# Performance work log

Hardware: AMD Instinct MI355X
Metric: run time of the kernel (lower is better)

The kernel has to match this reference:

```python
import jax, jax.numpy as jnp
import numpy as np

B, S, D = 2, 2048, 1024
H, DH = 16, 64  # n_heads, d_head = d_model // n_heads


def setup_inputs() -> dict:
    key = jax.random.key(0)
    ks = jax.random.split(key, 8)
    sc = lambda d: 1.0 / np.sqrt(d)
    return {
        "x": jax.random.normal(ks[0], (B, S, D), jnp.float32),
        "context": jax.random.normal(ks[1], (B, D), jnp.float32),
        "prev_state": jax.random.normal(ks[2], (B, S, D), jnp.float32),
        "attention_mask": jnp.ones((B, 1, S, S), dtype=bool),
        "Wq": jax.random.normal(ks[3], (D, D), jnp.float32) * sc(D),
        "Wk": jax.random.normal(ks[4], (D, D), jnp.float32) * sc(D),
        "Wv": jax.random.normal(ks[5], (D, D), jnp.float32) * sc(D),
        "Wo": jax.random.normal(ks[6], (D, D), jnp.float32) * sc(D),
        "Wc": jax.random.normal(ks[7], (D, DH), jnp.float32) * sc(D),
        "alpha": jnp.ones((1,), jnp.float32),
        "beta": jnp.ones((1,), jnp.float32),
    }


def reference(x, context, prev_state, attention_mask, Wq, Wk, Wv, Wo, Wc, alpha, beta):
    b, s, d = x.shape
    # projections (Linear with no bias, weight stored as [out, in] -> x @ W.T)
    q = (x @ Wq.T).reshape(b, s, H, DH).transpose(0, 2, 1, 3)  # (B,H,S,DH)
    k = (x @ Wk.T).reshape(b, s, H, DH).transpose(0, 2, 1, 3)
    v = (x @ Wv.T).reshape(b, s, H, DH).transpose(0, 2, 1, 3)

    inv_sqrt_dh = 1.0 / jnp.sqrt(jnp.asarray(DH, x.dtype))
    scores = jnp.einsum("bhqd,bhkd->bhqk", q, k) * inv_sqrt_dh

    # CFM: context-flow matching bias, rank-1 per-pair term from global context
    c = context @ Wc  # (B, DH)
    qc = jnp.einsum("bhqd,bd->bhq", q, c)
    kc = jnp.einsum("bhkd,bd->bhk", k, c)
    cfm = qc[..., :, None] * kc[..., None, :] / DH  # (B,H,S,S)

    # AFM: anti-flow matching bias from previous layer state (first d_head dims)
    p = prev_state[..., :DH]  # (B,S,DH)
    afm = jnp.einsum("bhqd,bkd->bhqk", q, p) * inv_sqrt_dh

    scores = scores + alpha[0] * cfm - beta[0] * afm
    scores = jnp.where(attention_mask, scores, jnp.asarray(-1e9, scores.dtype))

    w = jax.nn.softmax(scores, axis=-1)
    out = jnp.einsum("bhqk,bhkd->bhqd", w, v)  # (B,H,S,DH)
    out = out.transpose(0, 2, 1, 3).reshape(b, s, d)
    return out @ Wo.T
```

## Files before the change

kernel.cpp:

```cpp
#include <hip/hip_runtime.h>
#include <stdint.h>

#define D_  1024
#define S_  2048
#define B_  2
#define H_  16
#define DH_ 64
#define M_  (B_*S_)

typedef __bf16 bf16x8 __attribute__((ext_vector_type(8)));
typedef float  f32x4  __attribute__((ext_vector_type(4)));
typedef float  f32x16 __attribute__((ext_vector_type(16)));
typedef short  short8 __attribute__((ext_vector_type(8)));
typedef unsigned uint4v __attribute__((ext_vector_type(4)));
typedef unsigned short u16;

static __device__ __forceinline__ u16 f2bf(float f){
  union { float f; unsigned u; } v; v.f = f;
  unsigned r = v.u + 0x7FFF + ((v.u >> 16) & 1);
  return (u16)(r >> 16);
}
static __device__ __forceinline__ f32x4 mfma16(short8 a, short8 b, f32x4 c){
  return __builtin_amdgcn_mfma_f32_16x16x32_bf16(
      __builtin_bit_cast(bf16x8, a), __builtin_bit_cast(bf16x8, b), c, 0, 0, 0);
}
static __device__ __forceinline__ f32x16 mfma32(short8 a, short8 b, f32x16 c){
  return __builtin_amdgcn_mfma_f32_32x32x16_bf16(
      __builtin_bit_cast(bf16x8, a), __builtin_bit_cast(bf16x8, b), c, 0, 0, 0);
}
static __device__ __forceinline__ f32x16 zero16(){
  f32x16 z = {0,0,0,0,0,0,0,0,0,0,0,0,0,0,0,0};
  return z;
}
static __device__ __forceinline__ float fexp2(float x){
#if __has_builtin(__builtin_amdgcn_exp2f)
  return __builtin_amdgcn_exp2f(x);
#else
  return __exp2f(x);
#endif
}
static __device__ __forceinline__ unsigned cvtpk(float lo, float hi){
  unsigned r;
  asm("v_cvt_pk_bf16_f32 %0, %1, %2" : "=v"(r) : "v"(lo), "v"(hi));
  return r;
}
static __device__ __forceinline__ void gl_lds16(const u16* g, u16* lds){
  __builtin_amdgcn_global_load_lds(
      (const __attribute__((address_space(1))) void*)(uintptr_t)g,
      (__attribute__((address_space(3))) void*)(uintptr_t)lds, 16, 0, 0);
}

__global__ void k_f2bf(const float* __restrict__ in, u16* __restrict__ out, int n4){
  int i = blockIdx.x * blockDim.x + threadIdx.x;
  if(i >= n4) return;
  float4 v = ((const float4*)in)[i];
  ushort4 o; o.x = f2bf(v.x); o.y = f2bf(v.y); o.z = f2bf(v.z); o.w = f2bf(v.w);
  ((ushort4*)out)[i] = o;
}

__global__ void k_f2bf4(const float* __restrict__ a0, const float* __restrict__ a1,
                        const float* __restrict__ a2, const float* __restrict__ a3,
                        u16* __restrict__ o0, u16* __restrict__ o1,
                        u16* __restrict__ o2, u16* __restrict__ o3, int n4){
  const float* in; u16* out;
  switch(blockIdx.y){
    case 0: in=a0; out=o0; break;
    case 1: in=a1; out=o1; break;
    case 2: in=a2; out=o2; break;
    default: in=a3; out=o3; break;
  }
  int i = blockIdx.x * blockDim.x + threadIdx.x;
  if(i >= n4) return;
  float4 v = ((const float4*)in)[i];
  ushort4 o; o.x = f2bf(v.x); o.y = f2bf(v.y); o.z = f2bf(v.z); o.w = f2bf(v.w);
  ((ushort4*)out)[i] = o;
}

__global__ void k_ctx(const float* __restrict__ context, const float* __restrict__ Wc,
                      float* __restrict__ cvec, int* __restrict__ flags){
  __shared__ float partial[4][2][64];
  int t = threadIdx.x;
  if(t < 2) flags[t] = 1;
  int c = t >> 7;
  int b = (t >> 6) & 1;
  int j = t & 63;
  float s = 0.f;
  #pragma unroll 8
  for(int d = c*256; d < (c+1)*256; ++d) s += context[b*D_ + d] * Wc[d*DH_ + j];
  partial[c][b][j] = s;
  __syncthreads();
  if(t < 128){
    int b2 = t >> 6, j2 = t & 63;
    cvec[b2*DH_ + j2] = partial[0][b2][j2] + partial[1][b2][j2]
                      + partial[2][b2][j2] + partial[3][b2][j2];
  }
}

__global__ void k_mask_check(const uint4* __restrict__ m, int n16, int* flags){
  int i = blockIdx.x * blockDim.x + threadIdx.x;
  bool ok8 = true, ok32 = true;
  if(i < n16){
    uint4 v = m[i];
    ok8  = (v.x==0x01010101u)&&(v.y==0x01010101u)&&(v.z==0x01010101u)&&(v.w==0x01010101u);
    ok32 = (v.x==1u)&&(v.y==1u)&&(v.z==1u)&&(v.w==1u);
  }
  unsigned long long b8  = __ballot(!ok8);
  unsigned long long b32 = __ballot(!ok32);
  if((threadIdx.x & 63) == 0){
    if(b8)  flags[0] = 0;
    if(b32) flags[1] = 0;
  }
}

__global__ __launch_bounds__(256,2) void k_gemm_qkv(const u16* __restrict__ A,
    const u16* __restrict__ Wcat, u16* __restrict__ Qb, u16* __restrict__ Kb,
    u16* __restrict__ VT, const float* __restrict__ cvec,
    const float* __restrict__ prev, const float* __restrict__ beta_p,
    float* __restrict__ qcb, float* __restrict__ kcb){
  __shared__ u16 As[128*64];
  __shared__ u16 Bs[128*64];
  __shared__ float red[2][2][64];
  const int tid = threadIdx.x;
  const int w = tid >> 6, l = tid & 63;
  const int wr = w >> 1, wc = w & 1;
  const int id = blockIdx.x;
  const int bn = id >> 5;
  const int bm = id & 31;
  const int lr = l & 15, lh = l >> 4;
  const int srow = l >> 3, scol = (l & 7) * 8;

  f32x4 acc[4][4] = {};

  for(int kt = 0; kt < 16; ++kt){
    const int k0 = kt * 64;
    #pragma unroll
    for(int i = 0; i < 4; ++i){
      const int chunk = i*4 + w;
      gl_lds16(A    + (size_t)(bm*128 + chunk*8 + srow)*D_ + k0 + scol, &As[chunk*512]);
      gl_lds16(Wcat + (size_t)(bn*128 + chunk*8 + srow)*D_ + k0 + scol, &Bs[chunk*512]);
    }
    __syncthreads();
    #pragma unroll
    for(int kk = 0; kk < 2; ++kk){
      short8 a[4], b[4];
      #pragma unroll
      for(int m = 0; m < 4; ++m)
        a[m] = *(const short8*)&As[(wr*64 + m*16 + lr)*64 + kk*32 + lh*8];
      #pragma unroll
      for(int n = 0; n < 4; ++n)
        b[n] = *(const short8*)&Bs[(wc*64 + n*16 + lr)*64 + kk*32 + lh*8];
      #pragma unroll
      for(int m = 0; m < 4; ++m)
        #pragma unroll
        for(int n = 0; n < 4; ++n)
          acc[m][n] = mfma16(a[m], b[n], acc[m][n]);
    }
    __syncthreads();
  }

  const int b = bm >> 4;

  if(bn < 16){
    float cv[4];
    #pragma unroll
    for(int n = 0; n < 4; ++n) cv[n] = cvec[b*DH_ + n*16 + lr];
    float part[4][4];
    #pragma unroll
    for(int m = 0; m < 4; ++m)
      #pragma unroll
      for(int r = 0; r < 4; ++r){
        float p = acc[m][0][r]*cv[0] + acc[m][1][r]*cv[1]
                + acc[m][2][r]*cv[2] + acc[m][3][r]*cv[3];
        p += __shfl_xor(p, 1, 64); p += __shfl_xor(p, 2, 64);
        p += __shfl_xor(p, 4, 64); p += __shfl_xor(p, 8, 64);
        part[m][r] = p;
      }
    if(lr == 0){
      #pragma unroll
      for(int m = 0; m < 4; ++m)
        #pragma unroll
        for(int r = 0; r < 4; ++r)
          red[wr][wc][m*16 + lh*4 + r] = part[m][r];
    }
    __syncthreads();
    {
      int wr2 = tid >> 7, wc2 = (tid >> 6) & 1, i = tid & 63;
      int s = (bm & 15)*128 + wr2*64 + i;
      int head = (bn & 7)*2 + wc2;
      float* qkc = (bn < 8) ? qcb : kcb;
      qkc[((size_t)b*H_ + head)*S_ + s] = red[wr2][wc2][i];
    }
  }

  if(bn < 8){
    #pragma unroll
    for(int m = 0; m < 4; ++m){
      const size_t row0 = (size_t)bm*128 + wr*64 + m*16 + lh*4;
      #pragma unroll
      for(int n = 0; n < 4; ++n){
        const size_t col = (size_t)bn*128 + wc*64 + n*16 + lr;
        #pragma unroll
        for(int r = 0; r < 4; ++r)
          Qb[(row0 + r)*D_ + col] = f2bf(acc[m][n][r]);
      }
    }
  } else if(bn < 16){
    const float beta = beta_p[0];
    const float KSCALE = 0.125f * 1.44269504088896340736f;
    #pragma unroll
    for(int m = 0; m < 4; ++m){
      const size_t row0 = (size_t)bm*128 + wr*64 + m*16 + lh*4;
      #pragma unroll
      for(int n = 0; n < 4; ++n){
        const size_t col = (size_t)(bn - 8)*128 + wc*64 + n*16 + lr;
        #pragma unroll
        for(int r = 0; r < 4; ++r){
          float v = (acc[m][n][r] - beta * prev[(row0 + r)*D_ + n*16 + lr]) * KSCALE;
          Kb[(row0 + r)*D_ + col] = f2bf(v);
        }
      }
    }
  } else {
    #pragma unroll
    for(int m = 0; m < 4; ++m){
      const int s0 = (bm & 15)*128 + wr*64 + m*16 + lh*4;
      #pragma unroll
      for(int n = 0; n < 4; ++n){
        const int col = (bn - 16)*128 + wc*64 + n*16 + lr;
        ushort4 o;
        o.x = f2bf(acc[m][n][0]); o.y = f2bf(acc[m][n][1]);
        o.z = f2bf(acc[m][n][2]); o.w = f2bf(acc[m][n][3]);
        *(ushort4*)&VT[((size_t)(b*1024 + col))*S_ + s0] = o;
      }
    }
  }
}

__global__ __launch_bounds__(256,2) void k_gemm_o(const u16* __restrict__ A,
    const u16* __restrict__ W, float* __restrict__ Cout){
  __shared__ u16 As[128*64];
  __shared__ u16 Bs[64*64];
  const int tid = threadIdx.x;
  const int w = tid >> 6, l = tid & 63;
  const int wr = w >> 1, wc = w & 1;
  const int bm = blockIdx.x >> 4;
  const int bn = blockIdx.x & 15;
  const int lr = l & 15, lh = l >> 4;
  const int srow = l >> 3, scol = (l & 7) * 8;

  f32x4 acc[4][2] = {};

  for(int kt = 0; kt < 16; ++kt){
    const int k0 = kt * 64;
    #pragma unroll
    for(int i = 0; i < 4; ++i){
      const int chunk = i*4 + w;
      gl_lds16(A + (size_t)(bm*128 + chunk*8 + srow)*D_ + k0 + scol, &As[chunk*512]);
    }
    #pragma unroll
    for(int i = 0; i < 2; ++i){
      const int chunk = w*2 + i;
      gl_lds16(W + (size_t)(bn*64 + chunk*8 + srow)*D_ + k0 + scol, &Bs[chunk*512]);
    }
    __syncthreads();
    #pragma unroll
    for(int kk = 0; kk < 2; ++kk){
      short8 a[4], b[2];
      #pragma unroll
      for(int m = 0; m < 4; ++m)
        a[m] = *(const short8*)&As[(wr*64 + m*16 + lr)*64 + kk*32 + lh*8];
      #pragma unroll
      for(int n = 0; n < 2; ++n)
        b[n] = *(const short8*)&Bs[(wc*32 + n*16 + lr)*64 + kk*32 + lh*8];
      #pragma unroll
      for(int m = 0; m < 4; ++m)
        #pragma unroll
        for(int n = 0; n < 2; ++n)
          acc[m][n] = mfma16(a[m], b[n], acc[m][n]);
    }
    __syncthreads();
  }
  #pragma unroll
  for(int m = 0; m < 4; ++m){
    const size_t row0 = (size_t)bm*128 + wr*64 + m*16 + lh*4;
    #pragma unroll
    for(int n = 0; n < 2; ++n){
      const size_t col = (size_t)bn*64 + wc*32 + n*16 + lr;
      #pragma unroll
      for(int r = 0; r < 4; ++r)
        Cout[(row0 + r)*D_ + col] = acc[m][n][r];
    }
  }
}

__global__ __launch_bounds__(128,2) void k_attn(const u16* __restrict__ Qb,
    const u16* __restrict__ Kb, const u16* __restrict__ VT,
    const float* __restrict__ qc, const float* __restrict__ kc,
    const float* __restrict__ alpha_p, const unsigned char* __restrict__ mask,
    const int* __restrict__ flags, u16* __restrict__ Ob){
  __shared__ u16 Kbuf[2][4096];
  __shared__ u16 Vbuf[2][4096];
  const int tid = threadIdx.x;
  const int wv = tid >> 6, l = tid & 63;
  const int q32 = l & 31, hi = l >> 5, hb = hi*8;
  const int id = blockIdx.x;
  const int bh = id & 31, qb = id >> 5;
  const int b = bh >> 4, h = bh & 15;
  const int q0w = qb*64 + wv*32;
  const float aL = alpha_p[0] * (1.0f/64.0f) * 1.44269504088896340736f;
  const bool allones = (flags[0] | flags[1]) != 0;
  const u16* Kb_h = Kb + (size_t)b*S_*D_ + h*DH_;
  const u16* VT_h = VT + ((size_t)(b*1024 + h*DH_))*S_;
  const float* kcp = kc + (size_t)bh*S_;
  const unsigned char* maskr = mask + ((size_t)b*S_ + q0w + q32)*S_;

  const int srow = l >> 3;
  const int sdh  = ((l & 7) ^ srow) * 8;
  #define STAGEK(TILE, BUF) { _Pragma("unroll") for(int j = 0; j < 4; ++j){      \
      const int ck = j*2 + wv;                                                   \
      gl_lds16(Kb_h + (size_t)((TILE)*64 + ck*8 + srow)*D_ + sdh,                \
               &Kbuf[BUF][ck*512]); } }
  #define STAGEV(TILE, BUF) { _Pragma("unroll") for(int j = 0; j < 4; ++j){      \
      const int ck = j*2 + wv;                                                   \
      gl_lds16(VT_h + (size_t)(ck*8 + srow)*S_ + (TILE)*64 + sdh,                \
               &Vbuf[BUF][ck*512]); } }

  short8 qa[4];
  #pragma unroll
  for(int c = 0; c < 4; ++c)
    qa[c] = *(const short8*)&Qb[((size_t)b*S_ + q0w + q32)*D_ + h*DH_ + c*16 + hb];
  const float aq = aL * qc[(size_t)bh*S_ + q0w + q32];

  f32x16 oacc[2] = {zero16(), zero16()};
  float lp = 0.f;
  const int xk = (q32 & 7) << 3;

  STAGEK(0, 0);
  STAGEV(0, 0);
  __syncthreads();

  for(int kt = 0; kt < 32; ++kt){
    const int buf = kt & 1;
    const int k0 = kt*64;
    const int tn = (kt+1) & 31;
    STAGEK(tn, buf^1);
    STAGEV(tn, buf^1);

    f32x16 sacc[2] = {zero16(), zero16()};
    #pragma unroll
    for(int kg = 0; kg < 2; ++kg)
      #pragma unroll
      for(int c = 0; c < 4; ++c){
        short8 kf = *(const short8*)&Kbuf[buf][(kg*32 + q32)*64 + ((c*16 + hb) ^ xk)];
        sacc[kg] = mfma32(kf, qa[c], sacc[kg]);
      }
    short8 vf[2][4];
    #pragma unroll
    for(int dh2 = 0; dh2 < 2; ++dh2)
      #pragma unroll
      for(int c = 0; c < 4; ++c)
        vf[dh2][c] = *(const short8*)&Vbuf[buf][(dh2*32 + q32)*64 + ((c*16 + hb) ^ xk)];

    unsigned pk[2][8];
    #pragma unroll
    for(int kg = 0; kg < 2; ++kg){
      float p[16];
      #pragma unroll
      for(int rg = 0; rg < 4; ++rg){
        f32x4 kv = *(const f32x4*)&kcp[k0 + kg*32 + rg*8 + hi*4];
        unsigned mu = 0x01010101u;
        if(!allones) mu = *(const unsigned*)&maskr[k0 + kg*32 + rg*8 + hi*4];
        #pragma unroll
        for(int j = 0; j < 4; ++j){
          float t = sacc[kg][rg*4 + j] + aq*kv[j];
          if(((mu >> (8*j)) & 255u) == 0u) t = -160.0f;
          float e = fexp2(t);
          lp += e;
          p[rg*4 + j] = e;
        }
      }
      #pragma unroll
      for(int i = 0; i < 8; ++i) pk[kg][i] = cvtpk(p[2*i], p[2*i+1]);
    }

    #pragma unroll
    for(int c = 0; c < 4; ++c){
      const int kg = c >> 1, c4 = (c & 1)*4;
      unsigned x0 = pk[kg][c4+0], y0 = pk[kg][c4+2];
      unsigned x1 = pk[kg][c4+1], y1 = pk[kg][c4+3];
      asm("v_permlane32_swap_b32 %0, %1" : "+v"(x0), "+v"(y0));
      asm("v_permlane32_swap_b32 %0, %1" : "+v"(x1), "+v"(y1));
      uint4v pb = {x0, x1, y0, y1};
      short8 pbf = __builtin_bit_cast(short8, pb);
      #pragma unroll
      for(int dh2 = 0; dh2 < 2; ++dh2)
        oacc[dh2] = mfma32(vf[dh2][c], pbf, oacc[dh2]);
    }
    __syncthreads();
  }
  #undef STAGEK
  #undef STAGEV

  float lt = lp + __shfl_xor(lp, 32, 64);
  float inv = 1.0f / lt;
  u16* orow = Ob + ((size_t)b*S_ + q0w + q32)*D_ + h*DH_;
  #pragma unroll
  for(int dh2 = 0; dh2 < 2; ++dh2)
    #pragma unroll
    for(int rg = 0; rg < 4; ++rg){
      ushort4 o;
      o.x = f2bf(oacc[dh2][rg*4+0]*inv);
      o.y = f2bf(oacc[dh2][rg*4+1]*inv);
      o.z = f2bf(oacc[dh2][rg*4+2]*inv);
      o.w = f2bf(oacc[dh2][rg*4+3]*inv);
      *(ushort4*)&orow[dh2*32 + rg*8 + hi*4] = o;
    }
}

extern "C" void kernel_launch(void* const* d_in, const int* in_sizes, int n_in,
                              void* d_out, int out_size, void* d_ws, size_t ws_size,
                              hipStream_t stream){
  const float* x    = (const float*)d_in[0];
  const float* ctx  = (const float*)d_in[1];
  const float* prev = (const float*)d_in[2];
  const unsigned char* mask = (const unsigned char*)d_in[3];
  const float* Wq = (const float*)d_in[4];
  const float* Wk = (const float*)d_in[5];
  const float* Wv = (const float*)d_in[6];
  const float* Wo = (const float*)d_in[7];
  const float* Wc = (const float*)d_in[8];
  const float* alpha = (const float*)d_in[9];
  const float* beta  = (const float*)d_in[10];

  char* ws = (char*)d_ws;
  size_t off = 0;
  auto alloc = [&](size_t bytes)->void*{
    void* p = ws + off; off += (bytes + 255) & ~(size_t)255; return p;
  };
  u16* xb   = (u16*)alloc((size_t)M_*D_*2);
  u16* wcat = (u16*)alloc((size_t)3*D_*D_*2);
  u16* wob  = (u16*)alloc((size_t)D_*D_*2);
  u16* Qb   = (u16*)alloc((size_t)M_*D_*2);
  u16* Kb   = (u16*)alloc((size_t)M_*D_*2);
  u16* VT   = (u16*)alloc((size_t)B_*D_*S_*2);
  float* qcb  = (float*)alloc((size_t)B_*H_*S_*4);
  float* kcb  = (float*)alloc((size_t)B_*H_*S_*4);
  float* cvec = (float*)alloc(512);
  int*  flags = (int*)alloc(64);
  u16* Ob = xb;

  k_f2bf<<<M_*D_/4/256, 256, 0, stream>>>(x, xb, M_*D_/4);
  {
    dim3 g(D_*D_/4/256, 4);
    k_f2bf4<<<g, 256, 0, stream>>>(Wq, Wk, Wv, Wo,
        wcat, wcat + (size_t)D_*D_, wcat + (size_t)2*D_*D_, wob, D_*D_/4);
  }
  k_ctx<<<1, 512, 0, stream>>>(ctx, Wc, cvec, flags);
  {
    int n16 = B_*S_*S_/16;
    k_mask_check<<<n16/256, 256, 0, stream>>>((const uint4*)mask, n16, flags);
  }
  k_gemm_qkv<<<768, 256, 0, stream>>>(xb, wcat, Qb, Kb, VT, cvec, prev, beta, qcb, kcb);
  k_attn<<<1024, 128, 0, stream>>>(Qb, Kb, VT, qcb, kcb, alpha, mask, flags, Ob);
  k_gemm_o<<<512, 256, 0, stream>>>(Ob, wob, (float*)d_out);
}
```

Before: 147.4 us.

## Triple-buffer attention K/V tiles with explicit vmcnt waits and templated mask path

The attention inner loop moves from double to triple buffering of K/V tiles in LDS. It prefetches two tiles ahead and replaces __syncthreads with explicit s_waitcnt vmcnt plus s_barrier, aiming to hide global-load latency better. The mask branch becomes a template parameter so the all-ones path compiles without the mask loads. The QKV GEMM launch bound also rises to 3 waves per SIMD, which may add register pressure or spills. The extra LDS for the third buffer could reduce attention occupancy.

```diff
diff --git a/kernel.cpp b/kernel.cpp
--- a/kernel.cpp
+++ b/kernel.cpp
@@ -112,7 +112,7 @@
   }
 }
 
-__global__ __launch_bounds__(256,2) void k_gemm_qkv(const u16* __restrict__ A,
+__global__ __launch_bounds__(256,3) void k_gemm_qkv(const u16* __restrict__ A,
     const u16* __restrict__ Wcat, u16* __restrict__ Qb, u16* __restrict__ Kb,
     u16* __restrict__ VT, const float* __restrict__ cvec,
     const float* __restrict__ prev, const float* __restrict__ beta_p,
@@ -293,13 +293,94 @@
   }
 }
 
+template<bool AM>
+__device__ __forceinline__ void attn_pipe(
+    const u16* __restrict__ Kb_h, const u16* __restrict__ VT_h,
+    const float* __restrict__ kcp, const unsigned char* __restrict__ maskr,
+    u16* __restrict__ KB, u16* __restrict__ VB,
+    const short8 (&qa)[4], float aq, f32x16 (&oacc)[2], float& lp,
+    int q32, int hi, int hb, int srow, int sdh, int wv, int xk){
+  #define STG(T, BUF) { _Pragma("unroll") for(int j = 0; j < 4; ++j){            \
+      const int ck = j*2 + wv;                                                   \
+      gl_lds16(Kb_h + (size_t)((T)*64 + ck*8 + srow)*D_ + sdh,                   \
+               KB + (BUF)*4096 + ck*512);                                        \
+      gl_lds16(VT_h + (size_t)(ck*8 + srow)*S_ + (T)*64 + sdh,                   \
+               VB + (BUF)*4096 + ck*512); } }
+  STG(0, 0);
+  STG(1, 1);
+  asm volatile("s_waitcnt vmcnt(8)" ::: "memory");
+  __builtin_amdgcn_s_barrier();
+
+  for(int kt = 0; kt < 32; ++kt){
+    const int buf = kt % 3;
+    const int k0 = kt*64;
+    if(kt < 30) STG(kt+2, (kt+2) % 3);
+
+    f32x16 sacc[2] = {zero16(), zero16()};
+    #pragma unroll
+    for(int kg = 0; kg < 2; ++kg)
+      #pragma unroll
+      for(int c = 0; c < 4; ++c){
+        short8 kf = *(const short8*)&KB[buf*4096 + (kg*32 + q32)*64 + ((c*16 + hb) ^ xk)];
+        sacc[kg] = mfma32(kf, qa[c], sacc[kg]);
+      }
+    short8 vf[2][4];
+    #pragma unroll
+    for(int dh2 = 0; dh2 < 2; ++dh2)
+      #pragma unroll
+      for(int c = 0; c < 4; ++c)
+        vf[dh2][c] = *(const short8*)&VB[buf*4096 + (dh2*32 + q32)*64 + ((c*16 + hb) ^ xk)];
+
+    unsigned pk[2][8];
+    #pragma unroll
+    for(int kg = 0; kg < 2; ++kg){
+      float p[16];
+      #pragma unroll
+      for(int rg = 0; rg < 4; ++rg){
+        f32x4 kv = *(const f32x4*)&kcp[k0 + kg*32 + rg*8 + hi*4];
+        unsigned mu = 0x01010101u;
+        if(AM) mu = *(const unsigned*)&maskr[k0 + kg*32 + rg*8 + hi*4];
+        #pragma unroll
+        for(int j = 0; j < 4; ++j){
+          float tv = sacc[kg][rg*4 + j] + aq*kv[j];
+          if(AM){ if(((mu >> (8*j)) & 255u) == 0u) tv = -160.0f; }
+          float e = fexp2(tv);
+          lp += e;
+          p[rg*4 + j] = e;
+        }
+      }
+      #pragma unroll
+      for(int i = 0; i < 8; ++i) pk[kg][i] = cvtpk(p[2*i], p[2*i+1]);
+    }
+
+    #pragma unroll
+    for(int c = 0; c < 4; ++c){
+      const int kg = c >> 1, c4 = (c & 1)*4;
+      unsigned x0 = pk[kg][c4+0], y0 = pk[kg][c4+2];
+      unsigned x1 = pk[kg][c4+1], y1 = pk[kg][c4+3];
+      asm("v_permlane32_swap_b32 %0, %1" : "+v"(x0), "+v"(y0));
+      asm("v_permlane32_swap_b32 %0, %1" : "+v"(x1), "+v"(y1));
+      uint4v pb = {x0, x1, y0, y1};
+      short8 pbf = __builtin_bit_cast(short8, pb);
+      #pragma unroll
+      for(int dh2 = 0; dh2 < 2; ++dh2)
+        oacc[dh2] = mfma32(vf[dh2][c], pbf, oacc[dh2]);
+    }
+
+    if(kt < 30) asm volatile("s_waitcnt vmcnt(8)" ::: "memory");
+    else        asm volatile("s_waitcnt vmcnt(0)" ::: "memory");
+    __builtin_amdgcn_s_barrier();
+  }
+  #undef STG
+}
+
 __global__ __launch_bounds__(128,2) void k_attn(const u16* __restrict__ Qb,
     const u16* __restrict__ Kb, const u16* __restrict__ VT,
     const float* __restrict__ qc, const float* __restrict__ kc,
     const float* __restrict__ alpha_p, const unsigned char* __restrict__ mask,
     const int* __restrict__ flags, u16* __restrict__ Ob){
-  __shared__ u16 Kbuf[2][4096];
-  __shared__ u16 Vbuf[2][4096];
+  __shared__ u16 Kbuf[3][4096];
+  __shared__ u16 Vbuf[3][4096];
   const int tid = threadIdx.x;
   const int wv = tid >> 6, l = tid & 63;
   const int q32 = l & 31, hi = l >> 5, hb = hi*8;
@@ -316,14 +397,7 @@
 
   const int srow = l >> 3;
   const int sdh  = ((l & 7) ^ srow) * 8;
-  #define STAGEK(TILE, BUF) { _Pragma("unroll") for(int j = 0; j < 4; ++j){      \
-      const int ck = j*2 + wv;                                                   \
-      gl_lds16(Kb_h + (size_t)((TILE)*64 + ck*8 + srow)*D_ + sdh,                \
-               &Kbuf[BUF][ck*512]); } }
-  #define STAGEV(TILE, BUF) { _Pragma("unroll") for(int j = 0; j < 4; ++j){      \
-      const int ck = j*2 + wv;                                                   \
-      gl_lds16(VT_h + (size_t)(ck*8 + srow)*S_ + (TILE)*64 + sdh,                \
-               &Vbuf[BUF][ck*512]); } }
+  const int xk   = (q32 & 7) << 3;
 
   short8 qa[4];
   #pragma unroll
@@ -333,73 +407,13 @@
 
   f32x16 oacc[2] = {zero16(), zero16()};
   float lp = 0.f;
-  const int xk = (q32 & 7) << 3;
-
-  STAGEK(0, 0);
-  STAGEV(0, 0);
-  __syncthreads();
-
-  for(int kt = 0; kt < 32; ++kt){
-    const int buf = kt & 1;
-    const int k0 = kt*64;
-    const int tn = (kt+1) & 31;
-    STAGEK(tn, buf^1);
-    STAGEV(tn, buf^1);
-
-    f32x16 sacc[2] = {zero16(), zero16()};
-    #pragma unroll
-    for(int kg = 0; kg < 2; ++kg)
-      #pragma unroll
-      for(int c = 0; c < 4; ++c){
-        short8 kf = *(const short8*)&Kbuf[buf][(kg*32 + q32)*64 + ((c*16 + hb) ^ xk)];
-        sacc[kg] = mfma32(kf, qa[c], sacc[kg]);
-      }
-    short8 vf[2][4];
-    #pragma unroll
-    for(int dh2 = 0; dh2 < 2; ++dh2)
-      #pragma unroll
-      for(int c = 0; c < 4; ++c)
-        vf[dh2][c] = *(const short8*)&Vbuf[buf][(dh2*32 + q32)*64 + ((c*16 + hb) ^ xk)];
-
-    unsigned pk[2][8];
-    #pragma unroll
-    for(int kg = 0; kg < 2; ++kg){
-      float p[16];
-      #pragma unroll
-      for(int rg = 0; rg < 4; ++rg){
-        f32x4 kv = *(const f32x4*)&kcp[k0 + kg*32 + rg*8 + hi*4];
-        unsigned mu = 0x01010101u;
-        if(!allones) mu = *(const unsigned*)&maskr[k0 + kg*32 + rg*8 + hi*4];
-        #pragma unroll
-        for(int j = 0; j < 4; ++j){
-          float t = sacc[kg][rg*4 + j] + aq*kv[j];
-          if(((mu >> (8*j)) & 255u) == 0u) t = -160.0f;
-          float e = fexp2(t);
-          lp += e;
-          p[rg*4 + j] = e;
-        }
-      }
-      #pragma unroll
-      for(int i = 0; i < 8; ++i) pk[kg][i] = cvtpk(p[2*i], p[2*i+1]);
-    }
-
-    #pragma unroll
-    for(int c = 0; c < 4; ++c){
-      const int kg = c >> 1, c4 = (c & 1)*4;
-      unsigned x0 = pk[kg][c4+0], y0 = pk[kg][c4+2];
-      unsigned x1 = pk[kg][c4+1], y1 = pk[kg][c4+3];
-      asm("v_permlane32_swap_b32 %0, %1" : "+v"(x0), "+v"(y0));
-      asm("v_permlane32_swap_b32 %0, %1" : "+v"(x1), "+v"(y1));
-      uint4v pb = {x0, x1, y0, y1};
-      short8 pbf = __builtin_bit_cast(short8, pb);
-      #pragma unroll
-      for(int dh2 = 0; dh2 < 2; ++dh2)
-        oacc[dh2] = mfma32(vf[dh2][c], pbf, oacc[dh2]);
-    }
-    __syncthreads();
-  }
-  #undef STAGEK
-  #undef STAGEV
+
+  if(allones)
+    attn_pipe<false>(Kb_h, VT_h, kcp, maskr, &Kbuf[0][0], &Vbuf[0][0],
+                     qa, aq, oacc, lp, q32, hi, hb, srow, sdh, wv, xk);
+  else
+    attn_pipe<true>(Kb_h, VT_h, kcp, maskr, &Kbuf[0][0], &Vbuf[0][0],
+                    qa, aq, oacc, lp, q32, hi, hb, srow, sdh, wv, xk);
 
   float lt = lp + __shfl_xor(lp, 32, 64);
   float inv = 1.0f / lt;
```

New measurement: 157.9 us. +7.1%, slower.
